# Performance work log

Hardware: AMD Instinct MI355X
Metric: run time of the kernel (lower is better)

## Reference

```python
import jax, jax.numpy as jnp
import numpy as np

NUM_LEVELS = 4
RADIUS = 4


def _avg_pool2(x):
    # x: [B,S,C,H,W] -> 2x2 average pool, stride 2
    B, S, C, H, W = x.shape
    return x.reshape(B, S, C, H // 2, 2, W // 2, 2).mean(axis=(4, 6))


def _bilinear_sample(corr, x, y):
    # corr: [B,S,N,H,W]; x,y: [B,S,N,K,K] pixel coords; zeros padding, align_corners=True
    B, S, N, H, W = corr.shape
    corr_flat = corr.reshape(B, S, N, H * W)
    x0f = jnp.floor(x)
    y0f = jnp.floor(y)
    x0 = x0f.astype(jnp.int32)
    y0 = y0f.astype(jnp.int32)
    x1 = x0 + 1
    y1 = y0 + 1
    wx1 = x - x0f
    wx0 = 1.0 - wx1
    wy1 = y - y0f
    wy0 = 1.0 - wy1

    def gather(ix, iy):
        valid = ((ix >= 0) & (ix < W) & (iy >= 0) & (iy < H)).astype(corr.dtype)
        idx = jnp.clip(iy, 0, H - 1) * W + jnp.clip(ix, 0, W - 1)
        flat_idx = idx.reshape(B, S, N, -1)
        v = jnp.take_along_axis(corr_flat, flat_idx, axis=-1).reshape(ix.shape)
        return v * valid

    return (gather(x0, y0) * wx0 * wy0 + gather(x1, y0) * wx1 * wy0 +
            gather(x0, y1) * wx0 * wy1 + gather(x1, y1) * wx1 * wy1)


def _forward(features, targets, coordinates):
    B, S, C, H, W = features.shape
    N = targets.shape[2]
    inv_sqrt_c = 1.0 / jnp.sqrt(jnp.asarray(C, jnp.float32))

    # build feature pyramid
    pyramid = [features]
    f = features
    for _ in range(NUM_LEVELS - 1):
        f = _avg_pool2(f)
        pyramid.append(f)

    # correlate + windowed sample per level
    K = 2 * RADIUS + 1
    d = jnp.linspace(-RADIUS, RADIUS, K, dtype=jnp.float32)
    # faithful to torch: stack(meshgrid(dy, dx, indexing='ij'), -1)
    dyy, dxx = jnp.meshgrid(d, d, indexing='ij')
    delta = jnp.stack([dyy, dxx], axis=-1)  # [K,K,2]

    out_pyramid = []
    for i, feats in enumerate(pyramid):
        _, _, _, Hi, Wi = feats.shape
        # correlation volume [B,S,N,Hi,Wi]
        corr = jnp.einsum('bsnc,bschw->bsnhw', targets, feats) * inv_sqrt_c
        # window centers at this level
        centroid = coordinates[:, :, :, None, None, :] / (2.0 ** i)  # [B,S,N,1,1,2]
        pts = centroid + delta  # [B,S,N,K,K,2]; [...,0]=x, [...,1]=y (split order in torch code)
        sampled = _bilinear_sample(corr, pts[..., 0], pts[..., 1])  # [B,S,N,K,K]
        out_pyramid.append(sampled.reshape(B, S, N, K * K))

    return jnp.concatenate(out_pyramid, axis=-1)  # [B,S,N,NUM_LEVELS*K*K]


def setup_inputs() -> dict:
    key = jax.random.key(0)
    k1, k2, k3 = jax.random.split(key, 3)
    B, S, C, H, W = 1, 2, 128, 64, 96
    N = H * W
    features = jax.random.normal(k1, (B, S, C, H, W), dtype=jnp.float32)
    targets = jax.random.normal(k2, (B, S, N, C), dtype=jnp.float32)
    u = jax.random.uniform(k3, (B, S, N, 2), dtype=jnp.float32)
    scale = jnp.asarray([W - 1, H - 1], jnp.float32)  # x in [0,W-1], y in [0,H-1]
    coordinates = u * scale
    return {"features": features, "targets": targets, "coordinates": coordinates}


def reference(features, targets, coordinates):
    return _forward(features, targets, coordinates)
```

## Files before the change

kernel.cpp:

```cpp
#include <hip/hip_runtime.h>
#include <hip/hip_bf16.h>

#define SDIM 2
#define NPT  6144
#define CDIM 128
#define H0   64
#define W0   96

typedef __fp16 half2_t __attribute__((ext_vector_type(2)));

__constant__ int c_lvl_off[4] = {0, 786432, 983040, 1032192};

__device__ __forceinline__ unsigned pack_f16(float a, float b) {
    half2_t h = __builtin_amdgcn_cvt_pkrtz(a, b);
    return __builtin_bit_cast(unsigned, h);
}

__device__ __forceinline__ half2_t as_h2(unsigned u) {
    return __builtin_bit_cast(half2_t, u);
}

__global__ __launch_bounds__(256) void transpose_kernel(const float* __restrict__ feat,
                                                        unsigned* __restrict__ out) {
    __shared__ float lds[64 * 129];
    const int bid = blockIdx.x;
    const int s = bid / 96;
    const int p0 = (bid % 96) * 64;
    const int tid = threadIdx.x;
    const int sub = tid >> 6;
    const int lane = tid & 63;
#pragma unroll
    for (int k = 0; k < 32; ++k) {
        int c = sub + k * 4;
        lds[lane * 129 + c] = feat[(s * CDIM + c) * (H0 * W0) + p0 + lane];
    }
    __syncthreads();
#pragma unroll
    for (int k = 0; k < 16; ++k) {
        int pl = sub + k * 4;
        float lo = lds[pl * 129 + lane * 2];
        float hi = lds[pl * 129 + lane * 2 + 1];
        out[(size_t)(s * (H0 * W0) + p0 + pl) * 64 + lane] = pack_f16(lo, hi);
    }
}

__global__ __launch_bounds__(256) void pool_all_kernel(const unsigned* __restrict__ pyr0,
                                                       unsigned* __restrict__ pyr) {
    int idx = blockIdx.x * 256 + threadIdx.x;
    int lvl, rem;
    if (idx < 196608)      { lvl = 1; rem = idx; }
    else if (idx < 245760) { lvl = 2; rem = idx - 196608; }
    else if (idx < 258048) { lvl = 3; rem = idx - 245760; }
    else return;

    const int m = 1 << lvl;
    const int Wi = W0 >> lvl;
    const int Hi = H0 >> lvl;
    const int cp = rem & 63;
    const int pix = rem >> 6;
    const int x = pix % Wi;
    const int t = pix / Wi;
    const int y = t % Hi;
    const int s = t / Hi;

    const int row_stride = W0 * 64;
    const unsigned* base = pyr0 + ((s * H0 + y * m) * W0 + x * m) * 64 + cp;

    float lo = 0.0f, hi = 0.0f;
    for (int dy = 0; dy < m; ++dy) {
        const unsigned* rp = base + dy * row_stride;
        for (int dx = 0; dx < m; ++dx) {
            half2_t v = as_h2(rp[dx * 64]);
            lo += (float)v.x;
            hi += (float)v.y;
        }
    }
    const float inv = 1.0f / (float)(m * m);
    pyr[c_lvl_off[lvl] + rem] = pack_f16(lo * inv, hi * inv);
}

__global__ __launch_bounds__(256) void corr_kernel(const float* __restrict__ targets,
                                                   const float* __restrict__ coords,
                                                   const unsigned* __restrict__ pyr,
                                                   float* __restrict__ out) {
    __shared__ __align__(16) float tgt[CDIM];
    __shared__ float Ds[4][112];

    const int bid = blockIdx.x;
    const int xcd = bid & 7;
    const int s = xcd >> 2;
    const int sn = s * NPT + (bid >> 3) * 4 + (xcd & 3);
    const int tid = threadIdx.x;

    if (tid < CDIM) tgt[tid] = targets[(size_t)sn * CDIM + tid];
    const float cx = coords[sn * 2 + 0];
    const float cy = coords[sn * 2 + 1];
    __syncthreads();

    const int lvl = tid >> 6;
    const int lane = tid & 63;
    const int g = lane >> 2;
    const int k = lane & 3;

    const int Wi = W0 >> lvl;
    const int Hi = H0 >> lvl;
    const unsigned* base = pyr + c_lvl_off[lvl] + s * Hi * Wi * 64;

    const float scale = 1.0f / (float)(1 << lvl);
    const float cxl = cx * scale, cyl = cy * scale;
    const float x0f = floorf(cxl), y0f = floorf(cyl);
    const float wx1 = cxl - x0f, wx0 = 1.0f - wx1;
    const float wy1 = cyl - y0f, wy0 = 1.0f - wy1;
    const int ix0 = (int)x0f - 4;
    const int iy0 = (int)y0f - 4;

    half2_t treg[16];
#pragma unroll
    for (int q = 0; q < 16; ++q)
        treg[q] = __builtin_amdgcn_cvt_pkrtz(tgt[k * 32 + 2 * q], tgt[k * 32 + 2 * q + 1]);

    for (int it = 0; it < 7; ++it) {
        int p = it * 16 + g;
        if (p < 100) {
            int row = (p * 205) >> 11;
            int col = p - row * 10;
            int y = iy0 + row;
            int x = ix0 + col;
            bool valid = ((unsigned)x < (unsigned)Wi) && ((unsigned)y < (unsigned)Hi);
            int xc = min(max(x, 0), Wi - 1);
            int yc = min(max(y, 0), Hi - 1);
            const uint4* ptr = (const uint4*)(base + (yc * Wi + xc) * 64 + k * 16);
            float acc0 = 0.0f, acc1 = 0.0f;
#pragma unroll
            for (int q = 0; q < 4; ++q) {
                uint4 v = ptr[q];
                acc0 = __builtin_amdgcn_fdot2(as_h2(v.x), treg[q * 4 + 0], acc0, false);
                acc1 = __builtin_amdgcn_fdot2(as_h2(v.y), treg[q * 4 + 1], acc1, false);
                acc0 = __builtin_amdgcn_fdot2(as_h2(v.z), treg[q * 4 + 2], acc0, false);
                acc1 = __builtin_amdgcn_fdot2(as_h2(v.w), treg[q * 4 + 3], acc1, false);
            }
            float acc = acc0 + acc1;
            acc += __shfl_xor(acc, 1);
            acc += __shfl_xor(acc, 2);
            if (k == 0) Ds[lvl][p] = valid ? acc : 0.0f;
        }
    }

    __syncthreads();

    const float isc = 0.08838834764831843f;
    const size_t obase = (size_t)sn * 324 + lvl * 81;
#pragma unroll
    for (int r = 0; r < 2; ++r) {
        int o = r * 64 + lane;
        if (o < 81) {
            int j = (o * 57) >> 9;
            int i = o - j * 9;
            float d00 = Ds[lvl][i * 10 + j];
            float d01 = Ds[lvl][i * 10 + j + 1];
            float d10 = Ds[lvl][(i + 1) * 10 + j];
            float d11 = Ds[lvl][(i + 1) * 10 + j + 1];
            float v = wy0 * (wx0 * d00 + wx1 * d01) + wy1 * (wx0 * d10 + wx1 * d11);
            out[obase + o] = v * isc;
        }
    }
}

extern "C" void kernel_launch(void* const* d_in, const int* in_sizes, int n_in,
                              void* d_out, int out_size, void* d_ws, size_t ws_size,
                              hipStream_t stream) {
    const float* features = (const float*)d_in[0];
    const float* targets  = (const float*)d_in[1];
    const float* coords   = (const float*)d_in[2];
    float* out = (float*)d_out;

    unsigned* pyr = (unsigned*)d_ws;

    transpose_kernel<<<SDIM * (H0 * W0 / 64), 256, 0, stream>>>(features, pyr);

    pool_all_kernel<<<(258048 + 255) / 256, 256, 0, stream>>>(pyr, pyr);

    corr_kernel<<<SDIM * NPT, 256, 0, stream>>>(targets, coords, pyr, out);
}
```

Before: 162.0 us.

## Merge transpose and pooling into one prep kernel pooling from fp32 source

```diff
diff --git a/kernel.cpp b/kernel.cpp
--- a/kernel.cpp
+++ b/kernel.cpp
@@ -20,33 +20,34 @@
     return __builtin_bit_cast(half2_t, u);
 }
 
-__global__ __launch_bounds__(256) void transpose_kernel(const float* __restrict__ feat,
-                                                        unsigned* __restrict__ out) {
-    __shared__ float lds[64 * 129];
+__global__ __launch_bounds__(256) void prep_kernel(const float* __restrict__ feat,
+                                                   unsigned* __restrict__ pyr) {
     const int bid = blockIdx.x;
-    const int s = bid / 96;
-    const int p0 = (bid % 96) * 64;
     const int tid = threadIdx.x;
-    const int sub = tid >> 6;
-    const int lane = tid & 63;
+
+    if (bid < 192) {
+        __shared__ float lds[64 * 129];
+        const int s = bid / 96;
+        const int p0 = (bid % 96) * 64;
+        const int sub = tid >> 6;
+        const int lane = tid & 63;
 #pragma unroll
-    for (int k = 0; k < 32; ++k) {
-        int c = sub + k * 4;
-        lds[lane * 129 + c] = feat[(s * CDIM + c) * (H0 * W0) + p0 + lane];
+        for (int k = 0; k < 32; ++k) {
+            int c = sub + k * 4;
+            lds[lane * 129 + c] = feat[(s * CDIM + c) * (H0 * W0) + p0 + lane];
+        }
+        __syncthreads();
+#pragma unroll
+        for (int k = 0; k < 16; ++k) {
+            int pl = sub + k * 4;
+            float lo = lds[pl * 129 + lane * 2];
+            float hi = lds[pl * 129 + lane * 2 + 1];
+            pyr[(size_t)(s * (H0 * W0) + p0 + pl) * 64 + lane] = pack_f16(lo, hi);
+        }
+        return;
     }
-    __syncthreads();
-#pragma unroll
-    for (int k = 0; k < 16; ++k) {
-        int pl = sub + k * 4;
-        float lo = lds[pl * 129 + lane * 2];
-        float hi = lds[pl * 129 + lane * 2 + 1];
-        out[(size_t)(s * (H0 * W0) + p0 + pl) * 64 + lane] = pack_f16(lo, hi);
-    }
-}
 
-__global__ __launch_bounds__(256) void pool_all_kernel(const unsigned* __restrict__ pyr0,
-                                                       unsigned* __restrict__ pyr) {
-    int idx = blockIdx.x * 256 + threadIdx.x;
+    int idx = (bid - 192) * 256 + tid;
     int lvl, rem;
     if (idx < 196608)      { lvl = 1; rem = idx; }
     else if (idx < 245760) { lvl = 2; rem = idx - 196608; }
@@ -63,16 +64,14 @@
     const int y = t % Hi;
     const int s = t / Hi;
 
-    const int row_stride = W0 * 64;
-    const unsigned* base = pyr0 + ((s * H0 + y * m) * W0 + x * m) * 64 + cp;
-
+    const int c0 = 2 * cp;
     float lo = 0.0f, hi = 0.0f;
     for (int dy = 0; dy < m; ++dy) {
-        const unsigned* rp = base + dy * row_stride;
+        const float* r0 = feat + ((size_t)(s * CDIM + c0) * H0 + (y * m + dy)) * W0 + x * m;
+        const float* r1 = r0 + (size_t)H0 * W0;
         for (int dx = 0; dx < m; ++dx) {
-            half2_t v = as_h2(rp[dx * 64]);
-            lo += (float)v.x;
-            hi += (float)v.y;
+            lo += r0[dx];
+            hi += r1[dx];
         }
     }
     const float inv = 1.0f / (float)(m * m);
@@ -116,8 +115,12 @@
 
     half2_t treg[16];
 #pragma unroll
-    for (int q = 0; q < 16; ++q)
-        treg[q] = __builtin_amdgcn_cvt_pkrtz(tgt[k * 32 + 2 * q], tgt[k * 32 + 2 * q + 1]);
+    for (int q = 0; q < 4; ++q)
+#pragma unroll
+        for (int j = 0; j < 4; ++j) {
+            int c = q * 32 + k * 8 + 2 * j;
+            treg[q * 4 + j] = __builtin_amdgcn_cvt_pkrtz(tgt[c], tgt[c + 1]);
+        }
 
     for (int it = 0; it < 7; ++it) {
         int p = it * 16 + g;
@@ -129,11 +132,11 @@
             bool valid = ((unsigned)x < (unsigned)Wi) && ((unsigned)y < (unsigned)Hi);
             int xc = min(max(x, 0), Wi - 1);
             int yc = min(max(y, 0), Hi - 1);
-            const uint4* ptr = (const uint4*)(base + (yc * Wi + xc) * 64 + k * 16);
+            const uint4* pb = (const uint4*)(base + (yc * Wi + xc) * 64);
             float acc0 = 0.0f, acc1 = 0.0f;
 #pragma unroll
             for (int q = 0; q < 4; ++q) {
-                uint4 v = ptr[q];
+                uint4 v = pb[q * 4 + k];
                 acc0 = __builtin_amdgcn_fdot2(as_h2(v.x), treg[q * 4 + 0], acc0, false);
                 acc1 = __builtin_amdgcn_fdot2(as_h2(v.y), treg[q * 4 + 1], acc1, false);
                 acc0 = __builtin_amdgcn_fdot2(as_h2(v.z), treg[q * 4 + 2], acc0, false);
@@ -176,9 +179,7 @@
 
     unsigned* pyr = (unsigned*)d_ws;
 
-    transpose_kernel<<<SDIM * (H0 * W0 / 64), 256, 0, stream>>>(features, pyr);
-
-    pool_all_kernel<<<(258048 + 255) / 256, 256, 0, stream>>>(pyr, pyr);
+    prep_kernel<<<1200, 256, 0, stream>>>(features, pyr);
 
     corr_kernel<<<SDIM * NPT, 256, 0, stream>>>(targets, coords, pyr, out);
 }
```

Result: faster. 140.6 us (-13.2%).
